# Kernel tuning notes

Measured on AMD Instinct MI355X. Metric: run time of the kernel, lower is better.

Reference implementation:

```python
import jax, jax.numpy as jnp
import numpy as np

K = 0.1  # curvature (called k in the module)
EPS = 1e-15

def setup_inputs() -> dict:
    key = jax.random.key(0)
    k1, k2, k3 = jax.random.split(key, 3)
    B, C, D = 2048, 1000, 64
    x = jax.random.normal(k1, (B, D), dtype=jnp.float32) * 0.05  # inside ball
    a_vals = jax.random.normal(k2, (C, D), dtype=jnp.float32) * 0.05
    p_vals = jax.random.normal(k3, (C, D), dtype=jnp.float32) * 0.05
    return {"x": x, "a_vals": a_vals, "p_vals": p_vals}

def reference(x, a_vals, p_vals):
    k = jnp.asarray(K, dtype=x.dtype)
    sqrt_k = jnp.sqrt(k)
    # poincare_exp0: exponential map at the origin
    p_norm = jnp.maximum(jnp.linalg.norm(p_vals, axis=1, keepdims=True), EPS)  # [C,1]
    p_poin = jnp.tanh(sqrt_k * p_norm) * p_vals / (sqrt_k * p_norm)            # [C,D]
    # conformal scaling of a (as written in the module: 1 + k*||p||^2)
    p2 = jnp.sum(p_poin * p_poin, axis=1)                                      # [C]
    a_poin = a_vals * (1.0 + k * p2)[:, None]                                  # [C,D]
    # hyperbolic softmax logits
    lam = 2.0 / (1.0 - k * p2)                                                 # [C]
    a_norm = jnp.maximum(jnp.linalg.norm(a_poin, axis=1), EPS)                 # [C]
    scale = lam * a_norm / sqrt_k                                              # [C]
    # mobius addition of (-p) (+) x, batched -> [C,B,D]
    mp = -p_poin                                                               # [C,D]
    xy = jnp.einsum('cd,bd->cb', mp, x)                                        # [C,B]
    x2 = jnp.sum(mp * mp, axis=-1)[:, None]                                    # [C,1]
    y2 = jnp.sum(x * x, axis=-1)[None, :]                                      # [1,B]
    num = ((1.0 + 2.0 * k * xy + k * y2)[..., None] * mp[:, None, :]
           + (1.0 - k * x2)[..., None] * x[None, :, :])                        # [C,B,D]
    den = 1.0 + 2.0 * k * xy + (k * k) * x2 * y2                               # [C,B]
    mob = num / den[..., None]                                                 # [C,B,D]
    numer = 2.0 * sqrt_k * jnp.einsum('cbd,cd->cb', mob, a_poin)               # [C,B]
    denom = a_norm[:, None] * (1.0 - k * jnp.sum(mob * mob, axis=-1))          # [C,B]
    logits = scale[:, None] * jnp.arcsinh(numer / denom)                       # [C,B]
    return logits.T                                                            # [B,C]
```

## Files before the change

kernel.cpp:

```cpp
#include <hip/hip_runtime.h>
#include <hip/hip_bf16.h>
#include <math.h>

#define KCURV  0.1f
#define KK     0.010000001f
#define SQRT_K 0.31622776601683794f
#define TWO_SQRT_K 0.6324555320336759f
#define INV_SQRT_K 3.1622776601683795f
#define TD 64
#define LDP 72

typedef __bf16  bf16x8  __attribute__((ext_vector_type(8)));
typedef float   f32x4   __attribute__((ext_vector_type(4)));

__device__ __forceinline__ unsigned short f2bf(float f) {
    __hip_bfloat16 h = __float2bfloat16(f);
    return *(unsigned short*)&h;
}

__global__ __launch_bounds__(256) void fused_mlr_kernel(
    const float* __restrict__ x,
    const float* __restrict__ a_vals,
    const float* __restrict__ p_vals,
    float* __restrict__ out, int B, int C)
{
    __shared__ unsigned short Pl[64 * LDP];
    __shared__ unsigned short Al[64 * LDP];
    __shared__ float scal[4][64];

    const int tid  = threadIdx.x;
    const int w    = tid >> 6;
    const int lane = tid & 63;
    const int m16  = lane & 15;
    const int quad = lane >> 4;
    const int cb   = blockIdx.x * 64;
    const int rb   = blockIdx.y * 64;
    int arow = rb + 16 * w + m16; if (arow >= B) arow = B - 1;

    float xv[2][8];
    #pragma unroll
    for (int step = 0; step < 2; ++step) {
        const int ko = quad * 8 + step * 32;
        const float* xr = x + (size_t)arow * TD + ko;
        *(float4*)&xv[step][0] = *(const float4*)xr;
        *(float4*)&xv[step][4] = *(const float4*)(xr + 4);
    }

    {
        const int ci = tid >> 2;
        const int q  = tid & 3;
        int c = cb + ci; if (c >= C) c = C - 1;
        const float* pr = p_vals + (size_t)c * TD + q * 16;
        const float* ar = a_vals + (size_t)c * TD + q * 16;
        float pv[16], av[16];
        #pragma unroll
        for (int m = 0; m < 4; ++m) {
            *(float4*)&pv[m * 4] = *(const float4*)(pr + m * 4);
            *(float4*)&av[m * 4] = *(const float4*)(ar + m * 4);
        }
        float s_pp = 0.f, s_aa = 0.f, s_pa = 0.f;
        #pragma unroll
        for (int u = 0; u < 16; ++u) {
            s_pp = fmaf(pv[u], pv[u], s_pp);
            s_aa = fmaf(av[u], av[u], s_aa);
            s_pa = fmaf(pv[u], av[u], s_pa);
        }
        s_pp += __shfl_xor(s_pp, 1, 64); s_pp += __shfl_xor(s_pp, 2, 64);
        s_aa += __shfl_xor(s_aa, 1, 64); s_aa += __shfl_xor(s_aa, 2, 64);
        s_pa += __shfl_xor(s_pa, 1, 64); s_pa += __shfl_xor(s_pa, 2, 64);

        float pn = sqrtf(s_pp); if (pn < 1e-15f) pn = 1e-15f;
        float arg = SQRT_K * pn;
        float e2 = __expf(2.0f * arg);
        float th = (e2 - 1.0f) * __builtin_amdgcn_rcpf(e2 + 1.0f);
        float factor = (arg > 1e-4f) ? th * __builtin_amdgcn_rcpf(arg)
                                     : 1.0f - 0.333333333f * arg * arg;
        float p2 = factor * factor * s_pp;
        float ca = 1.0f + KCURV * p2;
        float anorm = ca * sqrtf(s_aa); if (anorm < 1e-15f) anorm = 1e-15f;
        float lam = 2.0f * __builtin_amdgcn_rcpf(1.0f - KCURV * p2);
        if (q == 0) {
            scal[0][ci] = p2;
            scal[1][ci] = -factor * ca * s_pa;
            scal[2][ci] = anorm;
            scal[3][ci] = lam * anorm * INV_SQRT_K;
        }
        unsigned short ubp[16], uba[16];
        #pragma unroll
        for (int u = 0; u < 16; ++u) {
            ubp[u] = f2bf(-factor * pv[u]);
            uba[u] = f2bf(ca * av[u]);
        }
        unsigned short* dp = &Pl[ci * LDP + q * 16];
        unsigned short* da = &Al[ci * LDP + q * 16];
        *(ulonglong2*)dp       = *(const ulonglong2*)&ubp[0];
        *(ulonglong2*)(dp + 8) = *(const ulonglong2*)&ubp[8];
        *(ulonglong2*)da       = *(const ulonglong2*)&uba[0];
        *(ulonglong2*)(da + 8) = *(const ulonglong2*)&uba[8];
    }
    __syncthreads();

    bf16x8 bp[4][2], ba[4][2];
    #pragma unroll
    for (int step = 0; step < 2; ++step) {
        #pragma unroll
        for (int t = 0; t < 4; ++t) {
            const int off = (16 * t + m16) * LDP + quad * 8 + step * 32;
            bp[t][step] = *(const bf16x8*)&Pl[off];
            ba[t][step] = *(const bf16x8*)&Al[off];
        }
    }

    float s = 0.f;
    #pragma unroll
    for (int step = 0; step < 2; ++step)
        #pragma unroll
        for (int u = 0; u < 8; ++u) s = fmaf(xv[step][u], xv[step][u], s);
    s += __shfl_xor(s, 16, 64);
    s += __shfl_xor(s, 32, 64);
    float y2r[4];
    #pragma unroll
    for (int r = 0; r < 4; ++r) y2r[r] = __shfl(s, quad * 4 + r, 64);

    bf16x8 af[2];
    #pragma unroll
    for (int step = 0; step < 2; ++step) {
        union { unsigned short u[8]; bf16x8 v; } cv;
        #pragma unroll
        for (int u = 0; u < 8; ++u) cv.u[u] = f2bf(xv[step][u]);
        af[step] = cv.v;
    }

    f32x4 accP[4], accA[4];
    #pragma unroll
    for (int t = 0; t < 4; ++t) {
        accP[t] = (f32x4){0.f, 0.f, 0.f, 0.f};
        accA[t] = (f32x4){0.f, 0.f, 0.f, 0.f};
    }
    #pragma unroll
    for (int step = 0; step < 2; ++step) {
        #pragma unroll
        for (int t = 0; t < 4; ++t) {
            accP[t] = __builtin_amdgcn_mfma_f32_16x16x32_bf16(af[step], bp[t][step], accP[t], 0, 0, 0);
            accA[t] = __builtin_amdgcn_mfma_f32_16x16x32_bf16(af[step], ba[t][step], accA[t], 0, 0, 0);
        }
    }

    #pragma unroll
    for (int t = 0; t < 4; ++t) {
        const int cl = cb + 16 * t + m16;
        const int si = 16 * t + m16;
        const float x2 = scal[0][si], pa = scal[1][si];
        const float an = scal[2][si], sc = scal[3][si];
        const float beta = 1.0f - KCURV * x2;
        const float kkx2 = KK * x2;
        #pragma unroll
        for (int r = 0; r < 4; ++r) {
            const int gr = rb + 16 * w + quad * 4 + r;
            const float y2 = y2r[r];
            const float xy = accP[t][r];
            const float xa = accA[t][r];
            float t1    = fmaf(2.0f * KCURV, xy, 1.0f);
            float den   = fmaf(kkx2, y2, t1);
            float alpha = fmaf(KCURV, y2, t1);
            float g     = fmaf(alpha, pa, beta * xa);
            float M     = fmaf(alpha * alpha, x2,
                          fmaf(2.0f * alpha * beta, xy, beta * beta * y2));
            float dd    = fmaf(den, den, -KCURV * M);
            float z     = TWO_SQRT_K * g * den * __builtin_amdgcn_rcpf(an * dd);
            float lg    = sc * __logf(z + sqrtf(fmaf(z, z, 1.0f)));
            if (cl < C && gr < B) out[(size_t)gr * C + cl] = lg;
        }
    }
}

extern "C" void kernel_launch(void* const* d_in, const int* in_sizes, int n_in,
                              void* d_out, int out_size, void* d_ws, size_t ws_size,
                              hipStream_t stream) {
    const float* x      = (const float*)d_in[0];
    const float* a_vals = (const float*)d_in[1];
    const float* p_vals = (const float*)d_in[2];
    const int B = in_sizes[0] / TD;
    const int C = in_sizes[1] / TD;
    const int rowBlocks = (B + 63) / 64;
    const int clsBlocks = (C + 63) / 64;

    dim3 grid(clsBlocks, rowBlocks);
    fused_mlr_kernel<<<grid, dim3(256), 0, stream>>>(
        x, a_vals, p_vals, (float*)d_out, B, C);
}
```

Baseline: 65.18 us.

## Use 512-thread blocks over 128 rows and interleave MFMA with epilogue

Each block now has 8 waves covering 128 batch rows instead of 64, so the per-class preprocessing of p and a (norms, tanh scaling, bf16 conversion to LDS) is shared by twice as many rows and the grid has half as many blocks. The class prep is split over 8 threads per class with an extra shuffle step, and its global loads are issued before the x loads. The MFMA accumulation now runs per 16-class tile just ahead of that tile's epilogue, which shortens accumulator lifetimes and lowers register pressure. The cost is fewer blocks (about 16x16) on a large GPU, which could reduce occupancy or load balance.

```diff
diff --git a/kernel.cpp b/kernel.cpp
--- a/kernel.cpp
+++ b/kernel.cpp
@@ -18,7 +18,7 @@
     return *(unsigned short*)&h;
 }
 
-__global__ __launch_bounds__(256) void fused_mlr_kernel(
+__global__ __launch_bounds__(512) void fused_mlr_kernel(
     const float* __restrict__ x,
     const float* __restrict__ a_vals,
     const float* __restrict__ p_vals,
@@ -34,8 +34,19 @@
     const int m16  = lane & 15;
     const int quad = lane >> 4;
     const int cb   = blockIdx.x * 64;
-    const int rb   = blockIdx.y * 64;
+    const int rb   = blockIdx.y * 128;
     int arow = rb + 16 * w + m16; if (arow >= B) arow = B - 1;
+
+    const int ci = tid >> 3;
+    const int o  = tid & 7;
+    int c = cb + ci; if (c >= C) c = C - 1;
+    const float* pr = p_vals + (size_t)c * TD + o * 8;
+    const float* ar = a_vals + (size_t)c * TD + o * 8;
+    float pv[8], av[8];
+    *(float4*)&pv[0] = *(const float4*)pr;
+    *(float4*)&pv[4] = *(const float4*)(pr + 4);
+    *(float4*)&av[0] = *(const float4*)ar;
+    *(float4*)&av[4] = *(const float4*)(ar + 4);
 
     float xv[2][8];
     #pragma unroll
@@ -47,27 +58,19 @@
     }
 
     {
-        const int ci = tid >> 2;
-        const int q  = tid & 3;
-        int c = cb + ci; if (c >= C) c = C - 1;
-        const float* pr = p_vals + (size_t)c * TD + q * 16;
-        const float* ar = a_vals + (size_t)c * TD + q * 16;
-        float pv[16], av[16];
-        #pragma unroll
-        for (int m = 0; m < 4; ++m) {
-            *(float4*)&pv[m * 4] = *(const float4*)(pr + m * 4);
-            *(float4*)&av[m * 4] = *(const float4*)(ar + m * 4);
-        }
         float s_pp = 0.f, s_aa = 0.f, s_pa = 0.f;
         #pragma unroll
-        for (int u = 0; u < 16; ++u) {
+        for (int u = 0; u < 8; ++u) {
             s_pp = fmaf(pv[u], pv[u], s_pp);
             s_aa = fmaf(av[u], av[u], s_aa);
             s_pa = fmaf(pv[u], av[u], s_pa);
         }
-        s_pp += __shfl_xor(s_pp, 1, 64); s_pp += __shfl_xor(s_pp, 2, 64);
-        s_aa += __shfl_xor(s_aa, 1, 64); s_aa += __shfl_xor(s_aa, 2, 64);
-        s_pa += __shfl_xor(s_pa, 1, 64); s_pa += __shfl_xor(s_pa, 2, 64);
+        s_pp += __shfl_xor(s_pp, 1, 64); s_aa += __shfl_xor(s_aa, 1, 64);
+        s_pa += __shfl_xor(s_pa, 1, 64);
+        s_pp += __shfl_xor(s_pp, 2, 64); s_aa += __shfl_xor(s_aa, 2, 64);
+        s_pa += __shfl_xor(s_pa, 2, 64);
+        s_pp += __shfl_xor(s_pp, 4, 64); s_aa += __shfl_xor(s_aa, 4, 64);
+        s_pa += __shfl_xor(s_pa, 4, 64);
 
         float pn = sqrtf(s_pp); if (pn < 1e-15f) pn = 1e-15f;
         float arg = SQRT_K * pn;
@@ -79,37 +82,22 @@
         float ca = 1.0f + KCURV * p2;
         float anorm = ca * sqrtf(s_aa); if (anorm < 1e-15f) anorm = 1e-15f;
         float lam = 2.0f * __builtin_amdgcn_rcpf(1.0f - KCURV * p2);
-        if (q == 0) {
+        if (o == 0) {
             scal[0][ci] = p2;
             scal[1][ci] = -factor * ca * s_pa;
             scal[2][ci] = anorm;
             scal[3][ci] = lam * anorm * INV_SQRT_K;
         }
-        unsigned short ubp[16], uba[16];
+        union { unsigned short u[8]; bf16x8 v; } cp, da;
         #pragma unroll
-        for (int u = 0; u < 16; ++u) {
-            ubp[u] = f2bf(-factor * pv[u]);
-            uba[u] = f2bf(ca * av[u]);
+        for (int u = 0; u < 8; ++u) {
+            cp.u[u] = f2bf(-factor * pv[u]);
+            da.u[u] = f2bf(ca * av[u]);
         }
-        unsigned short* dp = &Pl[ci * LDP + q * 16];
-        unsigned short* da = &Al[ci * LDP + q * 16];
-        *(ulonglong2*)dp       = *(const ulonglong2*)&ubp[0];
-        *(ulonglong2*)(dp + 8) = *(const ulonglong2*)&ubp[8];
-        *(ulonglong2*)da       = *(const ulonglong2*)&uba[0];
-        *(ulonglong2*)(da + 8) = *(const ulonglong2*)&uba[8];
+        *(ulonglong2*)&Pl[ci * LDP + o * 8] = *(const ulonglong2*)&cp.u[0];
+        *(ulonglong2*)&Al[ci * LDP + o * 8] = *(const ulonglong2*)&da.u[0];
     }
     __syncthreads();
-
-    bf16x8 bp[4][2], ba[4][2];
-    #pragma unroll
-    for (int step = 0; step < 2; ++step) {
-        #pragma unroll
-        for (int t = 0; t < 4; ++t) {
-            const int off = (16 * t + m16) * LDP + quad * 8 + step * 32;
-            bp[t][step] = *(const bf16x8*)&Pl[off];
-            ba[t][step] = *(const bf16x8*)&Al[off];
-        }
-    }
 
     float s = 0.f;
     #pragma unroll
@@ -131,23 +119,21 @@
         af[step] = cv.v;
     }
 
-    f32x4 accP[4], accA[4];
     #pragma unroll
     for (int t = 0; t < 4; ++t) {
-        accP[t] = (f32x4){0.f, 0.f, 0.f, 0.f};
-        accA[t] = (f32x4){0.f, 0.f, 0.f, 0.f};
-    }
-    #pragma unroll
-    for (int step = 0; step < 2; ++step) {
-        #pragma unroll
-        for (int t = 0; t < 4; ++t) {
-            accP[t] = __builtin_amdgcn_mfma_f32_16x16x32_bf16(af[step], bp[t][step], accP[t], 0, 0, 0);
-            accA[t] = __builtin_amdgcn_mfma_f32_16x16x32_bf16(af[step], ba[t][step], accA[t], 0, 0, 0);
-        }
-    }
+        const int off = (16 * t + m16) * LDP + quad * 8;
+        bf16x8 bp0 = *(const bf16x8*)&Pl[off];
+        bf16x8 ba0 = *(const bf16x8*)&Al[off];
+        bf16x8 bp1 = *(const bf16x8*)&Pl[off + 32];
+        bf16x8 ba1 = *(const bf16x8*)&Al[off + 32];
 
-    #pragma unroll
-    for (int t = 0; t < 4; ++t) {
+        f32x4 accP = (f32x4){0.f, 0.f, 0.f, 0.f};
+        f32x4 accA = (f32x4){0.f, 0.f, 0.f, 0.f};
+        accP = __builtin_amdgcn_mfma_f32_16x16x32_bf16(af[0], bp0, accP, 0, 0, 0);
+        accA = __builtin_amdgcn_mfma_f32_16x16x32_bf16(af[0], ba0, accA, 0, 0, 0);
+        accP = __builtin_amdgcn_mfma_f32_16x16x32_bf16(af[1], bp1, accP, 0, 0, 0);
+        accA = __builtin_amdgcn_mfma_f32_16x16x32_bf16(af[1], ba1, accA, 0, 0, 0);
+
         const int cl = cb + 16 * t + m16;
         const int si = 16 * t + m16;
         const float x2 = scal[0][si], pa = scal[1][si];
@@ -158,8 +144,8 @@
         for (int r = 0; r < 4; ++r) {
             const int gr = rb + 16 * w + quad * 4 + r;
             const float y2 = y2r[r];
-            const float xy = accP[t][r];
-            const float xa = accA[t][r];
+            const float xy = accP[r];
+            const float xa = accA[r];
             float t1    = fmaf(2.0f * KCURV, xy, 1.0f);
             float den   = fmaf(kkx2, y2, t1);
             float alpha = fmaf(KCURV, y2, t1);
@@ -182,10 +168,10 @@
     const float* p_vals = (const float*)d_in[2];
     const int B = in_sizes[0] / TD;
     const int C = in_sizes[1] / TD;
-    const int rowBlocks = (B + 63) / 64;
+    const int rowBlocks = (B + 127) / 128;
     const int clsBlocks = (C + 63) / 64;
 
     dim3 grid(clsBlocks, rowBlocks);
-    fused_mlr_kernel<<<grid, dim3(256), 0, stream>>>(
+    fused_mlr_kernel<<<grid, dim3(512), 0, stream>>>(
         x, a_vals, p_vals, (float*)d_out, B, C);
 }
```

Result: no change. 64.13 us (-1.6%).
